# Performance work log

Hardware: AMD Instinct MI355X
Metric: run time of the kernel (lower is better)

## Reference

```python
import jax, jax.numpy as jnp
import numpy as np

CONF_THR = 0.2      # confidence_threshold default
NMS_THR = 0.45      # nms_threshold default
TARGET_ID = 0       # NAME2ID['person'] in COCO ordering
CLASS_OFFSET = 1e4  # per-class box offset so cross-class IoU == 0 (per-class NMS)
B, N, C = 4, 8192, 80


def setup_inputs() -> dict:
    key = jax.random.key(0)
    kxy, kwh, kobj, kcls = jax.random.split(key, 4)
    xy = jax.random.uniform(kxy, (B, N, 2)) * 600.0          # x1, y1
    wh = jax.random.uniform(kwh, (B, N, 2)) * 100.0 + 1.0    # box w, h
    boxes = jnp.concatenate([xy, xy + wh], axis=-1)           # x1 y1 x2 y2
    obj = jax.random.uniform(kobj, (B, N, 1))                 # objectness score
    clsp = jax.random.uniform(kcls, (B, N, C))                # class probs
    detection = jnp.concatenate([boxes, obj, clsp], axis=-1)  # [B, N, 5+C]
    return {"detection": detection}


def _pairwise_iou(b):
    # b: [N, 4] in x1y1x2y2
    area = (b[:, 2] - b[:, 0]) * (b[:, 3] - b[:, 1])
    lt = jnp.maximum(b[:, None, :2], b[None, :, :2])
    rb = jnp.minimum(b[:, None, 2:], b[None, :, 2:])
    wh = jnp.clip(rb - lt, 0.0)
    inter = wh[..., 0] * wh[..., 1]
    return inter / (area[:, None] + area[None, :] - inter + 1e-9)


def _nms_image(boxes, scores, classprobs, labels):
    # Fixed-shape, masked equivalent of the torch per-image filter+per-class NMS.
    valid = (scores > CONF_THR) & (labels == TARGET_ID)
    s = jnp.where(valid, scores, -1.0)
    order = jnp.argsort(-s)  # descending score (NMS visiting order)
    b = boxes[order]
    s = s[order]
    cp = classprobs[order]
    lb = labels[order]
    v = valid[order]
    # Offset boxes per class label -> IoU between different classes is 0,
    # which exactly reproduces the per-class NMS loop.
    ob = b + lb.astype(b.dtype)[:, None] * CLASS_OFFSET
    iou = _pairwise_iou(ob)  # [N, N]

    def step(keep, xs):
        row, i, vi = xs
        suppressed = jnp.any(keep & (row > NMS_THR))
        k = vi & jnp.logical_not(suppressed)
        return keep.at[i].set(k), k

    _, keep = jax.lax.scan(
        step, jnp.zeros(s.shape[0], dtype=bool), (iou, jnp.arange(s.shape[0]), v)
    )
    # Compact kept detections to the front (stable sort preserves descending score
    # order among kept boxes, matching the final argsort in torch).
    s_rank = jnp.where(keep, s, -1.0)
    final = jnp.argsort(-s_rank)
    kf = keep[final]
    m = kf.astype(b.dtype)
    out_boxes = b[final] * m[:, None]
    out_scores = jnp.where(kf, s[final], 0.0)
    out_classprobs = cp[final] * m
    out_labels = jnp.where(kf, lb[final], -1)
    return out_boxes, out_scores, out_classprobs, out_labels


def reference(detection):
    # split_detections
    boxes = detection[..., :4]           # [B, N, 4]
    scores = detection[..., 4]           # [B, N]
    cls = detection[..., 5:]             # [B, N, C]
    classprobs = jnp.max(cls, axis=-1)
    labels = jnp.argmax(cls, axis=-1)
    # filter_detections, batched over images
    return jax.vmap(_nms_image)(boxes, scores, classprobs, labels)
```

## Files before the change

### kernel.cpp

```cpp
#include <hip/hip_runtime.h>
#include <cstdint>
#include <cstddef>

typedef unsigned long long u64;

#define BB 4
#define NN 8192
#define NC 80
#define DSTRIDE 85
#define CAP 512
#define SCAP 256
#define CONF_THRF 0.2f
#define NMS_THRF 0.45f

__global__ __launch_bounds__(256) void scan_kernel(
    const float* __restrict__ det, float* __restrict__ out,
    int* __restrict__ counts, float* __restrict__ cand) {
  int g = blockIdx.x * 256 + threadIdx.x;
  int row = g >> 2, q = g & 3;
  int b = row >> 13, nidx = row & (NN - 1);
  const float* d = det + (size_t)row * DSTRIDE;

  if (g < BB * NN) out[(size_t)BB * NN * 6 + g] = -1.0f;

  float best = -1.0f; int barg = 0;
#pragma unroll
  for (int k = 0; k < 20; ++k) {
    int c = q + 4 * k;
    float v = d[5 + c];
    if (v > best) { best = v; barg = c; }
  }
#pragma unroll
  for (int off = 1; off <= 2; off <<= 1) {
    float ov = __shfl_xor(best, off);
    int   oa = __shfl_xor(barg, off);
    if (ov > best || (ov == best && oa < barg)) { best = ov; barg = oa; }
  }

  if (q == 0) {
    float score = d[4];
    if (score > CONF_THRF && barg == 0) {
      int slot = atomicAdd(&counts[b], 1);
      if (slot < CAP) {
        float* p = cand + ((size_t)b * CAP + slot) * 8;
        p[0] = d[0]; p[1] = d[1]; p[2] = d[2]; p[3] = d[3];
        p[4] = score; p[5] = best; p[6] = __int_as_float(nidx);
      }
    }
  }
}

__global__ __launch_bounds__(256) void nms_kernel(
    float* __restrict__ out,
    const int* __restrict__ counts, const float* __restrict__ cand) {
  __shared__ u64 keys[SCAP];
  __shared__ float sx1[SCAP], sy1[SCAP], sx2[SCAP], sy2[SCAP];
  __shared__ float sar[SCAP], ssc[SCAP], scp[SCAP];
  __shared__ u64 mat[SCAP][4];

  const int b = blockIdx.x, tid = threadIdx.x;
  int K = counts[b];
  if (K > SCAP) K = SCAP;
  if (K < 0) K = 0;

  float x1 = 0, y1 = 0, x2 = 0, y2 = 0, sc = 0, cp = 0;
  if (tid < K) {
    const float* p = cand + ((size_t)b * CAP + tid) * 8;
    x1 = p[0]; y1 = p[1]; x2 = p[2]; y2 = p[3]; sc = p[4]; cp = p[5];
    int idx = __float_as_int(p[6]);
    keys[tid] = ((u64)__float_as_uint(sc) << 32) |
                ((u64)(unsigned)(0xFFFF - idx) << 16) | (unsigned)tid;
  }
  __syncthreads();

  if (tid < K) {
    u64 mykey = keys[tid];
    int r = 0;
    for (int s = 0; s < K; ++s) r += (keys[s] > mykey) ? 1 : 0;
    sx1[r] = x1; sy1[r] = y1; sx2[r] = x2; sy2[r] = y2;
    sar[r] = (x2 - x1) * (y2 - y1);
    ssc[r] = sc; scp[r] = cp;
  }
  __syncthreads();

  const int W = (K + 63) >> 6;
  for (int t = tid; t < K * 4; t += 256) {
    int i = t >> 2, w = t & 3;
    u64 word = 0;
    if (w < W) {
      float ax1 = sx1[i], ay1 = sy1[i], ax2 = sx2[i], ay2 = sy2[i], aa = sar[i];
      int j0 = w * 64;
      int jend = min(K, j0 + 64);
      for (int j = max(j0, i + 1); j < jend; ++j) {
        float xx1 = fmaxf(ax1, sx1[j]);
        float yy1 = fmaxf(ay1, sy1[j]);
        float xx2 = fminf(ax2, sx2[j]);
        float yy2 = fminf(ay2, sy2[j]);
        float wi = fmaxf(xx2 - xx1, 0.f);
        float hi = fmaxf(yy2 - yy1, 0.f);
        float inter = wi * hi;
        float iou = inter / (aa + sar[j] - inter + 1e-9f);
        if (iou > NMS_THRF) word |= 1ull << (j - j0);
      }
    }
    mat[i][w] = word;
  }
  __syncthreads();

  u64 rem0 = 0, rem1 = 0, rem2 = 0, rem3 = 0;
  u64 kp0 = 0, kp1 = 0, kp2 = 0, kp3 = 0;
#define GREEDY_CHUNK(WW, REMW, KPW)                                        \
  for (int ii = 0; ii < 64; ++ii) {                                        \
    int i = (WW)*64 + ii;                                                  \
    if (i >= K) break;                                                     \
    u64 m0 = mat[i][0], m1 = mat[i][1], m2 = mat[i][2], m3 = mat[i][3];    \
    if (!((REMW >> ii) & 1ull)) {                                          \
      KPW |= 1ull << ii;                                                   \
      rem0 |= m0; rem1 |= m1; rem2 |= m2; rem3 |= m3;                      \
    }                                                                      \
  }
  GREEDY_CHUNK(0, rem0, kp0)
  GREEDY_CHUNK(1, rem1, kp1)
  GREEDY_CHUNK(2, rem2, kp2)
  GREEDY_CHUNK(3, rem3, kp3)
#undef GREEDY_CHUNK

  if (tid < K) {
    int wi = tid >> 6, bi = tid & 63;
    u64 kw = (wi == 0) ? kp0 : (wi == 1) ? kp1 : (wi == 2) ? kp2 : kp3;
    if ((kw >> bi) & 1ull) {
      int r = (wi > 0 ? __popcll(kp0) : 0) + (wi > 1 ? __popcll(kp1) : 0) +
              (wi > 2 ? __popcll(kp2) : 0) +
              __popcll(kw & ((1ull << bi) - 1ull));
      size_t o = (size_t)b * NN + r;
      reinterpret_cast<float4*>(out)[o] =
          make_float4(sx1[tid], sy1[tid], sx2[tid], sy2[tid]);
      out[(size_t)BB * NN * 4 + o] = ssc[tid];
      out[(size_t)BB * NN * 5 + o] = scp[tid];
      out[(size_t)BB * NN * 6 + o] = 0.0f;
    }
  }
}

extern "C" void kernel_launch(void* const* d_in, const int* in_sizes, int n_in,
                              void* d_out, int out_size, void* d_ws, size_t ws_size,
                              hipStream_t stream) {
  const float* det = (const float*)d_in[0];
  float* out = (float*)d_out;
  int* counts = (int*)d_ws;
  float* cand = (float*)((char*)d_ws + 256);

  hipMemsetAsync(d_ws, 0, 16, stream);
  hipMemsetAsync(out, 0, (size_t)BB * NN * 6 * sizeof(float), stream);

  scan_kernel<<<(BB * NN * 4) / 256, 256, 0, stream>>>(det, out, counts, cand);
  nms_kernel<<<BB, 256, 0, stream>>>(out, counts, cand);
}
```

Measured before the change: 86.90 us.

## Fold output init into scan kernel and compact candidates with per-block ballots

The two hipMemsetAsync calls are removed; the scan kernel now zeroes the output planes and writes the -1 labels itself, one 64-row slice per block. Global atomicAdd slot allocation is replaced by wave ballots plus a block-level prefix, so each block writes its candidates to its own region and stores a per-block count. The NMS kernel scans these 128 counts to gather candidates into shared memory. Class-prob and box reads now use float4 loads from rows with an 85-float stride, which are not 16-byte aligned and rely on the hardware tolerating unaligned vector loads.

```diff
diff --git a/kernel.cpp b/kernel.cpp
--- a/kernel.cpp
+++ b/kernel.cpp
@@ -6,29 +6,36 @@
 
 #define BB 4
 #define NN 8192
-#define NC 80
 #define DSTRIDE 85
-#define CAP 512
+#define RPB 64
+#define BPI 128
+#define NBLK (BB * BPI)
+#define RCAP 64
 #define SCAP 256
 #define CONF_THRF 0.2f
 #define NMS_THRF 0.45f
+#define PLANE (BB * NN)
 
 __global__ __launch_bounds__(256) void scan_kernel(
     const float* __restrict__ det, float* __restrict__ out,
     int* __restrict__ counts, float* __restrict__ cand) {
-  int g = blockIdx.x * 256 + threadIdx.x;
-  int row = g >> 2, q = g & 3;
-  int b = row >> 13, nidx = row & (NN - 1);
+  __shared__ int wcnt[4];
+  const int tid = threadIdx.x;
+  const int blk = blockIdx.x;
+  const int r = tid >> 2, q = tid & 3;
+  const int row = blk * RPB + r;
   const float* d = det + (size_t)row * DSTRIDE;
 
-  if (g < BB * NN) out[(size_t)BB * NN * 6 + g] = -1.0f;
-
   float best = -1.0f; int barg = 0;
+  const float* cb = d + 5 + 20 * q;
 #pragma unroll
-  for (int k = 0; k < 20; ++k) {
-    int c = q + 4 * k;
-    float v = d[5 + c];
-    if (v > best) { best = v; barg = c; }
+  for (int k = 0; k < 5; ++k) {
+    float4 v = *reinterpret_cast<const float4*>(cb + 4 * k);
+    int c0 = 20 * q + 4 * k;
+    if (v.x > best) { best = v.x; barg = c0; }
+    if (v.y > best) { best = v.y; barg = c0 + 1; }
+    if (v.z > best) { best = v.z; barg = c0 + 2; }
+    if (v.w > best) { best = v.w; barg = c0 + 3; }
   }
 #pragma unroll
   for (int off = 1; off <= 2; off <<= 1) {
@@ -37,49 +44,94 @@
     if (ov > best || (ov == best && oa < barg)) { best = ov; barg = oa; }
   }
 
+  float4 box = make_float4(0.f, 0.f, 0.f, 0.f);
+  float score = 0.f;
+  bool valid = false;
   if (q == 0) {
-    float score = d[4];
-    if (score > CONF_THRF && barg == 0) {
-      int slot = atomicAdd(&counts[b], 1);
-      if (slot < CAP) {
-        float* p = cand + ((size_t)b * CAP + slot) * 8;
-        p[0] = d[0]; p[1] = d[1]; p[2] = d[2]; p[3] = d[3];
-        p[4] = score; p[5] = best; p[6] = __int_as_float(nidx);
-      }
-    }
-  }
+    box = *reinterpret_cast<const float4*>(d);
+    score = d[4];
+    valid = (score > CONF_THRF) && (barg == 0);
+  }
+
+  const int base = blk * RPB;
+  if (tid < 64) {
+    reinterpret_cast<float4*>(out)[base + tid] = make_float4(0.f, 0.f, 0.f, 0.f);
+  } else if (tid < 128) {
+    out[(size_t)PLANE * 4 + base + (tid - 64)] = 0.f;
+  } else if (tid < 192) {
+    out[(size_t)PLANE * 5 + base + (tid - 128)] = 0.f;
+  } else {
+    out[(size_t)PLANE * 6 + base + (tid - 192)] = -1.0f;
+  }
+
+  u64 mask = __ballot(valid);
+  const int wave = tid >> 6, lane = tid & 63;
+  if (lane == 0) wcnt[wave] = __popcll(mask);
+  __syncthreads();
+  if (valid) {
+    int offw = (wave > 0 ? wcnt[0] : 0) + (wave > 1 ? wcnt[1] : 0) +
+               (wave > 2 ? wcnt[2] : 0);
+    int pos = __popcll(mask & ((1ull << lane) - 1ull));
+    float* p = cand + ((size_t)blk * RCAP + (offw + pos)) * 8;
+    reinterpret_cast<float4*>(p)[0] = box;
+    reinterpret_cast<float4*>(p)[1] =
+        make_float4(score, best, __int_as_float(row & (NN - 1)), 0.f);
+  }
+  if (tid == 0) counts[blk] = wcnt[0] + wcnt[1] + wcnt[2] + wcnt[3];
 }
 
 __global__ __launch_bounds__(256) void nms_kernel(
-    float* __restrict__ out,
-    const int* __restrict__ counts, const float* __restrict__ cand) {
+    float* __restrict__ out, const int* __restrict__ counts,
+    const float* __restrict__ cand) {
+  __shared__ int cnt[BPI];
+  __shared__ float ux1[SCAP], uy1[SCAP], ux2[SCAP], uy2[SCAP];
+  __shared__ float usc[SCAP], ucp[SCAP];
   __shared__ u64 keys[SCAP];
   __shared__ float sx1[SCAP], sy1[SCAP], sx2[SCAP], sy2[SCAP];
   __shared__ float sar[SCAP], ssc[SCAP], scp[SCAP];
   __shared__ u64 mat[SCAP][4];
 
   const int b = blockIdx.x, tid = threadIdx.x;
-  int K = counts[b];
+
+  int c0 = 0;
+  if (tid < BPI) { c0 = counts[b * BPI + tid]; cnt[tid] = c0; }
+  __syncthreads();
+  for (int s = 1; s < BPI; s <<= 1) {
+    int v = 0;
+    if (tid < BPI) { v = cnt[tid]; if (tid >= s) v += cnt[tid - s]; }
+    __syncthreads();
+    if (tid < BPI) cnt[tid] = v;
+    __syncthreads();
+  }
+  int K = cnt[BPI - 1];
   if (K > SCAP) K = SCAP;
-  if (K < 0) K = 0;
-
-  float x1 = 0, y1 = 0, x2 = 0, y2 = 0, sc = 0, cp = 0;
+
+  if (tid < BPI && c0 > 0) {
+    int off = cnt[tid] - c0;
+    const float4* p = reinterpret_cast<const float4*>(
+        cand + ((size_t)(b * BPI + tid)) * RCAP * 8);
+    for (int k = 0; k < c0; ++k) {
+      int o = off + k;
+      if (o < SCAP) {
+        float4 v0 = p[2 * k], v1 = p[2 * k + 1];
+        ux1[o] = v0.x; uy1[o] = v0.y; ux2[o] = v0.z; uy2[o] = v0.w;
+        usc[o] = v1.x; ucp[o] = v1.y;
+        int idx = __float_as_int(v1.z);
+        keys[o] = ((u64)__float_as_uint(v1.x) << 32) |
+                  ((u64)(unsigned)(0xFFFF - idx) << 16) | (unsigned)o;
+      }
+    }
+  }
+  __syncthreads();
+
   if (tid < K) {
-    const float* p = cand + ((size_t)b * CAP + tid) * 8;
-    x1 = p[0]; y1 = p[1]; x2 = p[2]; y2 = p[3]; sc = p[4]; cp = p[5];
-    int idx = __float_as_int(p[6]);
-    keys[tid] = ((u64)__float_as_uint(sc) << 32) |
-                ((u64)(unsigned)(0xFFFF - idx) << 16) | (unsigned)tid;
-  }
-  __syncthreads();
-
-  if (tid < K) {
-    u64 mykey = keys[tid];
+    u64 my = keys[tid];
     int r = 0;
-    for (int s = 0; s < K; ++s) r += (keys[s] > mykey) ? 1 : 0;
+    for (int s = 0; s < K; ++s) r += (keys[s] > my) ? 1 : 0;
+    float x1 = ux1[tid], y1 = uy1[tid], x2 = ux2[tid], y2 = uy2[tid];
     sx1[r] = x1; sy1[r] = y1; sx2[r] = x2; sy2[r] = y2;
     sar[r] = (x2 - x1) * (y2 - y1);
-    ssc[r] = sc; scp[r] = cp;
+    ssc[r] = usc[tid]; scp[r] = ucp[tid];
   }
   __syncthreads();
 
@@ -111,7 +163,7 @@
   u64 kp0 = 0, kp1 = 0, kp2 = 0, kp3 = 0;
 #define GREEDY_CHUNK(WW, REMW, KPW)                                        \
   for (int ii = 0; ii < 64; ++ii) {                                        \
-    int i = (WW)*64 + ii;                                                  \
+    int i = (WW) * 64 + ii;                                                \
     if (i >= K) break;                                                     \
     u64 m0 = mat[i][0], m1 = mat[i][1], m2 = mat[i][2], m3 = mat[i][3];    \
     if (!((REMW >> ii) & 1ull)) {                                          \
@@ -135,9 +187,9 @@
       size_t o = (size_t)b * NN + r;
       reinterpret_cast<float4*>(out)[o] =
           make_float4(sx1[tid], sy1[tid], sx2[tid], sy2[tid]);
-      out[(size_t)BB * NN * 4 + o] = ssc[tid];
-      out[(size_t)BB * NN * 5 + o] = scp[tid];
-      out[(size_t)BB * NN * 6 + o] = 0.0f;
+      out[(size_t)PLANE * 4 + o] = ssc[tid];
+      out[(size_t)PLANE * 5 + o] = scp[tid];
+      out[(size_t)PLANE * 6 + o] = 0.0f;
     }
   }
 }
@@ -148,11 +200,8 @@
   const float* det = (const float*)d_in[0];
   float* out = (float*)d_out;
   int* counts = (int*)d_ws;
-  float* cand = (float*)((char*)d_ws + 256);
-
-  hipMemsetAsync(d_ws, 0, 16, stream);
-  hipMemsetAsync(out, 0, (size_t)BB * NN * 6 * sizeof(float), stream);
-
-  scan_kernel<<<(BB * NN * 4) / 256, 256, 0, stream>>>(det, out, counts, cand);
+  float* cand = (float*)((char*)d_ws + 2048);
+
+  scan_kernel<<<NBLK, 256, 0, stream>>>(det, out, counts, cand);
   nms_kernel<<<BB, 256, 0, stream>>>(out, counts, cand);
 }
```

Measured after the change: 84.41 us. 2.9% less time.
